# Kernel optimization log

Hardware: AMD Instinct MI355X
Metric: run time of the kernel (lower is better)

Reference implementation:

```python
import jax, jax.numpy as jnp
import numpy as np

EPS = 1e-5


def grid_sample_bilinear_border(img, grid):
    """PyTorch F.grid_sample(mode='bilinear', padding_mode='border', align_corners=False).
    img: [B,C,H,W], grid: [B,Hg,Wg,2] with (x,y) in [-1,1]. Returns [B,C,Hg,Wg]."""
    B, C, H, W = img.shape
    gx, gy = grid[..., 0], grid[..., 1]
    # unnormalize (align_corners=False), then border-clamp the coordinate
    ix = jnp.clip((gx + 1.0) * (W * 0.5) - 0.5, 0.0, W - 1.0)
    iy = jnp.clip((gy + 1.0) * (H * 0.5) - 0.5, 0.0, H - 1.0)
    x0f = jnp.floor(ix)
    y0f = jnp.floor(iy)
    wx = ix - x0f  # [B,Hg,Wg]
    wy = iy - y0f
    x0 = jnp.clip(x0f.astype(jnp.int32), 0, W - 1)
    y0 = jnp.clip(y0f.astype(jnp.int32), 0, H - 1)
    x1 = jnp.clip(x0 + 1, 0, W - 1)
    y1 = jnp.clip(y0 + 1, 0, H - 1)

    def gather(im, y, x):  # im [C,H,W]; y,x [Hg,Wg] -> [C,Hg,Wg]
        return im[:, y, x]

    g = jax.vmap(gather)
    v00 = g(img, y0, x0)
    v01 = g(img, y0, x1)
    v10 = g(img, y1, x0)
    v11 = g(img, y1, x1)
    wx = wx[:, None]  # [B,1,Hg,Wg]
    wy = wy[:, None]
    return (v00 * (1 - wx) * (1 - wy) + v01 * wx * (1 - wy)
            + v10 * (1 - wx) * wy + v11 * wx * wy)


def bn_relu(x, gamma, beta, mean, var):
    # x: [B,Cc,N,H,W]; per-channel inference batchnorm + relu
    shape = (1, -1, 1, 1, 1)
    inv = gamma * jax.lax.rsqrt(var + EPS)
    return jax.nn.relu(x * inv.reshape(shape) + (beta - mean * inv).reshape(shape))


def setup_inputs() -> dict:
    key = jax.random.key(0)
    ks = jax.random.split(key, 16)
    B, C, H, W = 4, 64, 256, 320
    N, G = 9, 8
    return {
        "ref_feature": jax.random.normal(ks[0], (B, C, H, W), jnp.float32),
        "grid": jax.random.uniform(ks[1], (B, N * H, W, 2), jnp.float32, minval=-1.0, maxval=1.0),
        "conv0_w": jax.random.normal(ks[2], (16, G), jnp.float32) * 0.2,
        "bn0_gamma": jax.random.uniform(ks[3], (16,), jnp.float32, minval=0.5, maxval=1.5),
        "bn0_beta": jax.random.normal(ks[4], (16,), jnp.float32) * 0.1,
        "bn0_mean": jax.random.normal(ks[5], (16,), jnp.float32) * 0.1,
        "bn0_var": jax.random.uniform(ks[6], (16,), jnp.float32, minval=0.5, maxval=1.5),
        "conv1_w": jax.random.normal(ks[7], (8, 16), jnp.float32) * 0.2,
        "bn1_gamma": jax.random.uniform(ks[8], (8,), jnp.float32, minval=0.5, maxval=1.5),
        "bn1_beta": jax.random.normal(ks[9], (8,), jnp.float32) * 0.1,
        "bn1_mean": jax.random.normal(ks[10], (8,), jnp.float32) * 0.1,
        "bn1_var": jax.random.uniform(ks[11], (8,), jnp.float32, minval=0.5, maxval=1.5),
        "sim_w": jax.random.normal(ks[12], (1, 8), jnp.float32) * 0.2,
        "sim_b": jax.random.normal(ks[13], (1,), jnp.float32) * 0.1,
    }


def reference(ref_feature, grid, conv0_w, bn0_gamma, bn0_beta, bn0_mean, bn0_var,
              conv1_w, bn1_gamma, bn1_beta, bn1_mean, bn1_var, sim_w, sim_b):
    B, C, H, W = ref_feature.shape
    G = 8
    N = grid.shape[1] // H  # neighbors
    Cg = C // G
    # irregular bilinear gather: [B,C,N*H,W] -> [B,G,Cg,N,H,W]
    sampled = grid_sample_bilinear_border(ref_feature, grid).reshape(B, G, Cg, N, H, W)
    ref = ref_feature.reshape(B, G, Cg, H, W)[:, :, :, None]  # [B,G,Cg,1,H,W]
    weight = (sampled * ref).mean(axis=2)  # group similarity, [B,G,N,H,W]
    # 1x1x1 conv stack (conv-bn-relu x2, then conv + sigmoid)
    x = bn_relu(jnp.einsum('og,bgnhw->bonhw', conv0_w, weight),
                bn0_gamma, bn0_beta, bn0_mean, bn0_var)
    x = bn_relu(jnp.einsum('oc,bcnhw->bonhw', conv1_w, x),
                bn1_gamma, bn1_beta, bn1_mean, bn1_var)
    sim = jnp.einsum('oc,bcnhw->bonhw', sim_w, x) + sim_b.reshape(1, -1, 1, 1, 1)
    return jax.nn.sigmoid(sim[:, 0])  # [B,N,H,W]
```

## Files before the change

### kernel.cpp

```cpp
#include <hip/hip_runtime.h>
#include <hip/hip_fp16.h>

#define B_ 4
#define C_ 64
#define H_ 256
#define W_ 320
#define N_ 9
#define TOT (B_*N_*H_*W_)
#define HW_ (H_*W_)
#define HWC (H_*W_*C_)
#define NPB (N_*HW_)

#define NHWC_HALFS (B_*H_*W_*C_)
#define PRM_OFF_BYTES (NHWC_HALFS*2)

union H2x4U { float4 f; __half2 h[4]; };

__global__ __launch_bounds__(512) void fold_params(
    const float* __restrict__ w0, const float* __restrict__ g0, const float* __restrict__ be0,
    const float* __restrict__ mu0, const float* __restrict__ va0,
    const float* __restrict__ w1, const float* __restrict__ g1, const float* __restrict__ be1,
    const float* __restrict__ mu1, const float* __restrict__ va1,
    const float* __restrict__ sw, const float* __restrict__ sb, float* __restrict__ prm)
{
    int t = threadIdx.x;
    if (t < 128) {
        int o = t >> 3;
        float a = g0[o] / sqrtf(va0[o] + 1e-5f);
        prm[t] = w0[t] * a;
    } else if (t < 144) {
        int o = t - 128;
        float a = g0[o] / sqrtf(va0[o] + 1e-5f);
        prm[128 + o] = be0[o] - mu0[o] * a;
    } else if (t < 272) {
        int i = t - 144;
        int c = i >> 4;
        float a = g1[c] / sqrtf(va1[c] + 1e-5f);
        prm[144 + i] = w1[i] * a;
    } else if (t < 280) {
        int c = t - 272;
        float a = g1[c] / sqrtf(va1[c] + 1e-5f);
        prm[272 + c] = be1[c] - mu1[c] * a;
    } else if (t < 288) {
        prm[t] = sw[t - 280];
    } else if (t == 288) {
        prm[288] = sb[0];
    }
}

__global__ __launch_bounds__(256) void nchw_to_nhwc_fp16(const float* __restrict__ in,
                                                         __half* __restrict__ out)
{
    __shared__ unsigned int tile[64 * 34];
    const int blk = blockIdx.x;
    const int b   = blk / (HW_ / 64);
    const int hw0 = (blk % (HW_ / 64)) * 64;
    const int tid = threadIdx.x;
    const int px  = tid & 63;
    const int q   = tid >> 6;

    const float* src = in + (size_t)b * HWC + hw0;
#pragma unroll
    for (int i = 0; i < 8; ++i) {
        int c = i * 8 + q * 2;
        float f0 = src[(size_t)c * HW_ + px];
        float f1 = src[(size_t)(c + 1) * HW_ + px];
        __half2 h = __floats2half2_rn(f0, f1);
        tile[px * 34 + (c >> 1)] = *(unsigned int*)&h;
    }
    __syncthreads();

    __half* dstbase = out + ((size_t)b * HW_ + hw0) * C_;
#pragma unroll
    for (int j = 0; j < 2; ++j) {
        int p  = j * 32 + (tid >> 3);
        int cg = tid & 7;
        const unsigned int* r = &tile[p * 34 + cg * 4];
        uint4 v;
        v.x = r[0]; v.y = r[1]; v.z = r[2]; v.w = r[3];
        *(uint4*)(dstbase + (size_t)p * C_ + cg * 8) = v;
    }
}

__device__ __forceinline__ __half2 bl_acc(__half2 a00, __half2 a01, __half2 a10, __half2 a11,
                                          __half2 r, __half2 wxh, __half2 wyh, __half2 acc)
{
    __half2 top = __hfma2(wxh, __hsub2(a01, a00), a00);
    __half2 bot = __hfma2(wxh, __hsub2(a11, a10), a10);
    __half2 s   = __hfma2(wyh, __hsub2(bot, top), top);
    return __hfma2(s, r, acc);
}

__device__ __forceinline__ float gd_compute(const H2x4U& r, const H2x4U& v00, const H2x4U& v01,
                                            const H2x4U& v10, const H2x4U& v11, float wx, float wy)
{
    __half2 wxh = __float2half2_rn(wx);
    __half2 wyh = __float2half2_rn(wy);
    __half2 acc = __float2half2_rn(0.f);
    acc = bl_acc(v00.h[0], v01.h[0], v10.h[0], v11.h[0], r.h[0], wxh, wyh, acc);
    acc = bl_acc(v00.h[1], v01.h[1], v10.h[1], v11.h[1], r.h[1], wxh, wyh, acc);
    acc = bl_acc(v00.h[2], v01.h[2], v10.h[2], v11.h[2], r.h[2], wxh, wyh, acc);
    acc = bl_acc(v00.h[3], v01.h[3], v10.h[3], v11.h[3], r.h[3], wxh, wyh, acc);
    float2 f = __half22float2(acc);
    return (f.x + f.y) * 0.125f;
}

__global__ __launch_bounds__(256, 5) void fwn_main(const __half* __restrict__ img,
                                                   const float* __restrict__ grid,
                                                   const float* __restrict__ prm,
                                                   float* __restrict__ out)
{
    __shared__ float wlds[256][9];
    __shared__ int   ash[256 * 9];
    const int tid  = threadIdx.x;
    const int lane = tid & 63;
    const int wv   = tid >> 6;
    const int g    = lane & 7;
    const int sub  = lane >> 3;
    const int g8   = g * 8;

    const int blk  = blockIdx.x;
    const int xcd  = blk & 7;
    const int b    = xcd >> 1;
    const int slab = ((blk >> 3) << 1) | (xcd & 1);
    const int hwb  = slab * 256;
    const int ibase = b * HWC;

    H2x4U refr[8];
#pragma unroll
    for (int pp = 0; pp < 8; ++pp) {
        int px = wv * 64 + pp * 8 + sub;
        refr[pp].f = *(const float4*)(img + ibase + (hwb + px) * C_ + g8);
    }

    const float2* gbase = (const float2*)grid + (size_t)b * NPB + hwb;
    float* obase = out + (size_t)b * NPB + hwb;

    for (int n = 0; n < N_; ++n) {
        {
            float2 gxy = gbase[n * HW_ + tid];
            float ix = fminf(fmaxf((gxy.x + 1.f) * (W_ * 0.5f) - 0.5f, 0.f), (float)(W_ - 1));
            float iy = fminf(fmaxf((gxy.y + 1.f) * (H_ * 0.5f) - 0.5f, 0.f), (float)(H_ - 1));
            float x0f = floorf(ix), y0f = floorf(iy);
            int x0 = (int)x0f, y0 = (int)y0f;
            int dx = (x0 < W_ - 1) ? C_ : 0;
            int dy = (y0 < H_ - 1) ? W_ * C_ : 0;
            int r9 = tid * 9;
            ash[r9 + 0] = ibase + (y0 * W_ + x0) * C_;
            ash[r9 + 1] = dx;
            ash[r9 + 2] = dy;
            ash[r9 + 3] = __float_as_int(ix - x0f);
            ash[r9 + 4] = __float_as_int(iy - y0f);
        }
        __syncthreads();

#pragma unroll
        for (int pp = 0; pp < 8; ++pp) {
            int px = wv * 64 + pp * 8 + sub;
            int r9 = px * 9;
            int o  = ash[r9 + 0] + g8;
            int dx = ash[r9 + 1];
            int dy = ash[r9 + 2];
            float wx = __int_as_float(ash[r9 + 3]);
            float wy = __int_as_float(ash[r9 + 4]);
            H2x4U v00, v01, v10, v11;
            v00.f = *(const float4*)(img + o);
            v01.f = *(const float4*)(img + o + dx);
            v10.f = *(const float4*)(img + o + dy);
            v11.f = *(const float4*)(img + o + dx + dy);
            wlds[px][g] = gd_compute(refr[pp], v00, v01, v10, v11, wx, wy);
        }
        __syncthreads();

        float wv8[8];
#pragma unroll
        for (int i = 0; i < 8; ++i) wv8[i] = wlds[tid][i];

        float h0[16];
#pragma unroll
        for (int o = 0; o < 16; ++o) {
            float a = prm[128 + o];
#pragma unroll
            for (int gg = 0; gg < 8; ++gg) a = fmaf(prm[o * 8 + gg], wv8[gg], a);
            h0[o] = fmaxf(a, 0.f);
        }
        float s = prm[288];
#pragma unroll
        for (int c = 0; c < 8; ++c) {
            float a = prm[272 + c];
#pragma unroll
            for (int o = 0; o < 16; ++o) a = fmaf(prm[144 + c * 16 + o], h0[o], a);
            float h1 = fmaxf(a, 0.f);
            s = fmaf(prm[280 + c], h1, s);
        }
        obase[n * HW_ + tid] = 1.f / (1.f + __expf(-s));
    }
}

extern "C" void kernel_launch(void* const* d_in, const int* in_sizes, int n_in,
                              void* d_out, int out_size, void* d_ws, size_t ws_size,
                              hipStream_t stream)
{
    const float* ref   = (const float*)d_in[0];
    const float* grd   = (const float*)d_in[1];
    const float* w0    = (const float*)d_in[2];
    const float* g0    = (const float*)d_in[3];
    const float* be0   = (const float*)d_in[4];
    const float* mu0   = (const float*)d_in[5];
    const float* va0   = (const float*)d_in[6];
    const float* w1    = (const float*)d_in[7];
    const float* g1    = (const float*)d_in[8];
    const float* be1   = (const float*)d_in[9];
    const float* mu1   = (const float*)d_in[10];
    const float* va1   = (const float*)d_in[11];
    const float* sw    = (const float*)d_in[12];
    const float* sb    = (const float*)d_in[13];
    float* out = (float*)d_out;

    __half* img = (__half*)d_ws;
    float* prm  = (float*)((char*)d_ws + PRM_OFF_BYTES);

    fold_params<<<1, 512, 0, stream>>>(w0, g0, be0, mu0, va0, w1, g1, be1, mu1, va1, sw, sb, prm);
    nchw_to_nhwc_fp16<<<B_ * (HW_ / 64), 256, 0, stream>>>(ref, img);
    fwn_main<<<B_ * (HW_ / 256), 256, 0, stream>>>(img, grd, prm, out);
}
```

Before: 313.1 us.

## Bucket block samples by source row band to improve gather locality

Each block now computes all 9 neighbor grid coordinates up front and packs offset, border flags and fp16 weights into compact records. A wave/block prefix scan then sorts the 2304 samples into four buckets by y0/64 row band, so each processing chunk gathers from nearby image rows. The reference feature is reloaded per sample instead of held in registers, and outputs are scattered back via a stored sample id. This costs extra LDS, scan work, extra reference loads, an extra barrier per chunk and lower occupancy (launch bound 5 to 4), in exchange for better cache locality on the random bilinear gathers.

```diff
diff --git a/kernel.cpp b/kernel.cpp
--- a/kernel.cpp
+++ b/kernel.cpp
@@ -10,6 +10,7 @@
 #define HW_ (H_*W_)
 #define HWC (H_*W_*C_)
 #define NPB (N_*HW_)
+#define SMP 2304
 
 #define NHWC_HALFS (B_*H_*W_*C_)
 #define PRM_OFF_BYTES (NHWC_HALFS*2)
@@ -105,13 +106,17 @@
     return (f.x + f.y) * 0.125f;
 }
 
-__global__ __launch_bounds__(256, 5) void fwn_main(const __half* __restrict__ img,
+__global__ __launch_bounds__(256, 4) void fwn_main(const __half* __restrict__ img,
                                                    const float* __restrict__ grid,
                                                    const float* __restrict__ prm,
                                                    float* __restrict__ out)
 {
+    __shared__ unsigned int recA[SMP];
+    __shared__ unsigned int recB[SMP];
+    __shared__ unsigned short sidA[SMP];
     __shared__ float wlds[256][9];
-    __shared__ int   ash[256 * 9];
+    __shared__ unsigned long long waveTot[4];
+
     const int tid  = threadIdx.x;
     const int lane = tid & 63;
     const int wv   = tid >> 6;
@@ -126,74 +131,117 @@
     const int hwb  = slab * 256;
     const int ibase = b * HWC;
 
-    H2x4U refr[8];
-#pragma unroll
-    for (int pp = 0; pp < 8; ++pp) {
-        int px = wv * 64 + pp * 8 + sub;
-        refr[pp].f = *(const float4*)(img + ibase + (hwb + px) * C_ + g8);
-    }
-
     const float2* gbase = (const float2*)grid + (size_t)b * NPB + hwb;
     float* obase = out + (size_t)b * NPB + hwb;
 
+    unsigned int w0s[9], w1s[9];
+    int ss[9];
+    unsigned int cnt[4] = {0, 0, 0, 0};
+#pragma unroll
     for (int n = 0; n < N_; ++n) {
-        {
-            float2 gxy = gbase[n * HW_ + tid];
-            float ix = fminf(fmaxf((gxy.x + 1.f) * (W_ * 0.5f) - 0.5f, 0.f), (float)(W_ - 1));
-            float iy = fminf(fmaxf((gxy.y + 1.f) * (H_ * 0.5f) - 0.5f, 0.f), (float)(H_ - 1));
-            float x0f = floorf(ix), y0f = floorf(iy);
-            int x0 = (int)x0f, y0 = (int)y0f;
-            int dx = (x0 < W_ - 1) ? C_ : 0;
-            int dy = (y0 < H_ - 1) ? W_ * C_ : 0;
-            int r9 = tid * 9;
-            ash[r9 + 0] = ibase + (y0 * W_ + x0) * C_;
-            ash[r9 + 1] = dx;
-            ash[r9 + 2] = dy;
-            ash[r9 + 3] = __float_as_int(ix - x0f);
-            ash[r9 + 4] = __float_as_int(iy - y0f);
-        }
-        __syncthreads();
-
+        float2 gxy = gbase[n * HW_ + tid];
+        float ix = fminf(fmaxf((gxy.x + 1.f) * (W_ * 0.5f) - 0.5f, 0.f), (float)(W_ - 1));
+        float iy = fminf(fmaxf((gxy.y + 1.f) * (H_ * 0.5f) - 0.5f, 0.f), (float)(H_ - 1));
+        float x0f = floorf(ix), y0f = floorf(iy);
+        int x0 = (int)x0f, y0 = (int)y0f;
+        unsigned int w0 = (unsigned int)((y0 * W_ + x0) * C_);
+        if (x0 < W_ - 1) w0 |= 1u << 23;
+        if (y0 < H_ - 1) w0 |= 1u << 24;
+        __half2 wxy = __floats2half2_rn(ix - x0f, iy - y0f);
+        w0s[n] = w0;
+        w1s[n] = *(unsigned int*)&wxy;
+        int st = y0 >> 6;
+        ss[n] = st;
+        cnt[st]++;
+    }
+
+    unsigned long long pk = (unsigned long long)cnt[0] | ((unsigned long long)cnt[1] << 16)
+                          | ((unsigned long long)cnt[2] << 32) | ((unsigned long long)cnt[3] << 48);
+    unsigned long long inc = pk;
+#pragma unroll
+    for (int d = 1; d < 64; d <<= 1) {
+        unsigned long long o = __shfl_up(inc, d, 64);
+        if (lane >= d) inc += o;
+    }
+    if (lane == 63) waveTot[wv] = inc;
+    __syncthreads();
+    unsigned long long wbase = 0, tot = 0;
+#pragma unroll
+    for (int w = 0; w < 4; ++w) {
+        unsigned long long t = waveTot[w];
+        if (w < wv) wbase += t;
+        tot += t;
+    }
+    unsigned int bbase[4];
+    bbase[0] = 0;
+    bbase[1] = (unsigned int)(tot & 0xFFFF);
+    bbase[2] = bbase[1] + (unsigned int)((tot >> 16) & 0xFFFF);
+    bbase[3] = bbase[2] + (unsigned int)((tot >> 32) & 0xFFFF);
+    unsigned long long excl = wbase + inc - pk;
+
+    unsigned int run[4] = {0, 0, 0, 0};
+#pragma unroll
+    for (int n = 0; n < N_; ++n) {
+        int st = ss[n];
+        unsigned int pos = bbase[st] + (unsigned int)((excl >> (16 * st)) & 0xFFFF) + run[st];
+        run[st]++;
+        recA[pos] = w0s[n];
+        recB[pos] = w1s[n];
+        sidA[pos] = (unsigned short)((n << 8) | tid);
+    }
+    __syncthreads();
+
+    for (int ch = 0; ch < 9; ++ch) {
 #pragma unroll
         for (int pp = 0; pp < 8; ++pp) {
-            int px = wv * 64 + pp * 8 + sub;
-            int r9 = px * 9;
-            int o  = ash[r9 + 0] + g8;
-            int dx = ash[r9 + 1];
-            int dy = ash[r9 + 2];
-            float wx = __int_as_float(ash[r9 + 3]);
-            float wy = __int_as_float(ash[r9 + 4]);
-            H2x4U v00, v01, v10, v11;
+            int lslot = wv * 64 + pp * 8 + sub;
+            int slot  = ch * 256 + lslot;
+            unsigned int w0 = recA[slot];
+            unsigned int w1 = recB[slot];
+            int sid = sidA[slot];
+            int o  = ibase + (int)(w0 & 0x7FFFFF) + g8;
+            int dx = (w0 & (1u << 23)) ? C_ : 0;
+            int dy = (w0 & (1u << 24)) ? W_ * C_ : 0;
+            __half2 wxy = *(__half2*)&w1;
+            float wx = __half2float(__low2half(wxy));
+            float wy = __half2float(__high2half(wxy));
+
+            H2x4U r_, v00, v01, v10, v11;
+            r_.f  = *(const float4*)(img + ibase + (hwb + (sid & 255)) * C_ + g8);
             v00.f = *(const float4*)(img + o);
             v01.f = *(const float4*)(img + o + dx);
             v10.f = *(const float4*)(img + o + dy);
             v11.f = *(const float4*)(img + o + dx + dy);
-            wlds[px][g] = gd_compute(refr[pp], v00, v01, v10, v11, wx, wy);
+            wlds[lslot][g] = gd_compute(r_, v00, v01, v10, v11, wx, wy);
         }
         __syncthreads();
 
-        float wv8[8];
-#pragma unroll
-        for (int i = 0; i < 8; ++i) wv8[i] = wlds[tid][i];
-
-        float h0[16];
-#pragma unroll
-        for (int o = 0; o < 16; ++o) {
-            float a = prm[128 + o];
-#pragma unroll
-            for (int gg = 0; gg < 8; ++gg) a = fmaf(prm[o * 8 + gg], wv8[gg], a);
-            h0[o] = fmaxf(a, 0.f);
+        {
+            int sid = sidA[ch * 256 + tid];
+            float wv8[8];
+#pragma unroll
+            for (int i = 0; i < 8; ++i) wv8[i] = wlds[tid][i];
+
+            float h0[16];
+#pragma unroll
+            for (int o = 0; o < 16; ++o) {
+                float a = prm[128 + o];
+#pragma unroll
+                for (int gg = 0; gg < 8; ++gg) a = fmaf(prm[o * 8 + gg], wv8[gg], a);
+                h0[o] = fmaxf(a, 0.f);
+            }
+            float s = prm[288];
+#pragma unroll
+            for (int c = 0; c < 8; ++c) {
+                float a = prm[272 + c];
+#pragma unroll
+                for (int o = 0; o < 16; ++o) a = fmaf(prm[144 + c * 16 + o], h0[o], a);
+                float h1 = fmaxf(a, 0.f);
+                s = fmaf(prm[280 + c], h1, s);
+            }
+            obase[(sid >> 8) * HW_ + (sid & 255)] = 1.f / (1.f + __expf(-s));
         }
-        float s = prm[288];
-#pragma unroll
-        for (int c = 0; c < 8; ++c) {
-            float a = prm[272 + c];
-#pragma unroll
-            for (int o = 0; o < 16; ++o) a = fmaf(prm[144 + c * 16 + o], h0[o], a);
-            float h1 = fmaxf(a, 0.f);
-            s = fmaf(prm[280 + c], h1, s);
-        }
-        obase[n * HW_ + tid] = 1.f / (1.f + __expf(-s));
+        __syncthreads();
     }
 }
 
```

Result: no change. 309.0 us (-1.3%).
